# Optimization experiments

Hardware: AMD Instinct MI355X
Metric: run time of the kernel (lower is better)

## Reference

```python
import jax, jax.numpy as jnp
import numpy as np

E, B, F, L = 4, 8192, 2048, 100  # envs, batch/env, feature dim, num classes
LAM = 1.0  # hparams['RERM_lam']


def setup_inputs() -> dict:
    key = jax.random.key(0)
    k1, k2, k3 = jax.random.split(key, 3)
    feats = jax.random.normal(k1, (E, B, F), jnp.float32)
    y = jax.random.randint(k2, (E, B), 0, L)
    W = jax.random.normal(k3, (F, L), jnp.float32) * 0.02
    b = jnp.zeros((L,), jnp.float32)
    return {"feats": feats, "y": y, "W": W, "b": b}


def _rerm_loss(feats, y, W, b):
    # --- per-(label, env) masked means (mean_table / visit_table) ---
    onehot = jax.nn.one_hot(y, L, dtype=feats.dtype)          # [E,B,L]
    counts = onehot.sum(axis=1)                               # [E,L]
    sums = jnp.einsum('ebl,ebf->elf', onehot, feats)          # [E,L,F]
    means = sums / jnp.maximum(counts, 1.0)[..., None]        # [E,L,F]
    visit = (counts > 0).astype(feats.dtype)                  # [E,L]

    # --- torch.var(mean_table[i, fetch_envs, :], dim=1): variance over
    # feature dim per env (unbiased, /(F-1)), then mean over visited envs ---
    mu = means.mean(axis=-1, keepdims=True)                   # [E,L,1]
    var = jnp.sum((means - mu) ** 2, axis=-1) / (F - 1)       # [E,L]

    nvis = visit.sum(axis=0)                                  # [L]
    sel = (nvis > 1.5).astype(feats.dtype)                    # labels with >1 env
    per_label = (var * visit).sum(axis=0) / jnp.maximum(nvis, 1.0)  # [L]
    nzlabel = jnp.maximum(sel.sum(), 1.0)
    mean_loss = LAM * jnp.sum(per_label * sel) / nzlabel

    # --- cross-entropy over all envs concatenated ---
    logits = feats.reshape(E * B, F) @ W + b                  # [E*B,L]
    logp = jax.nn.log_softmax(logits, axis=-1)
    ce = -jnp.take_along_axis(logp, y.reshape(-1, 1), axis=1).mean()

    return mean_loss + ce


def reference(feats, y, W, b):
    return _rerm_loss(feats, y, W, b)
```

## Files before the change

### kernel.cpp

```cpp
#include <hip/hip_runtime.h>
#include <hip/hip_bf16.h>
#include <math.h>

#define E 4
#define B 8192
#define F 2048
#define L 100
#define NROWS (E * B)
#define LAMBDA 1.0f

typedef __attribute__((ext_vector_type(8))) short bf16x8;
typedef __attribute__((ext_vector_type(4))) float f32x4;

static __device__ inline unsigned short f2bf(float x) {
    unsigned u = __float_as_uint(x);
    unsigned r = (u + 0x7FFFu + ((u >> 16) & 1u)) >> 16;
    return (unsigned short)r;
}

__global__ void __launch_bounds__(256) k_prep(const float* __restrict__ W,
                                              unsigned short* __restrict__ Wt) {
    int g = blockIdx.x * 256 + threadIdx.x;
    int n = g >> 9;
    int k = (g & 511) * 4;
    ushort4 v;
    if (n < L) {
        v.x = f2bf(W[(size_t)(k + 0) * L + n]);
        v.y = f2bf(W[(size_t)(k + 1) * L + n]);
        v.z = f2bf(W[(size_t)(k + 2) * L + n]);
        v.w = f2bf(W[(size_t)(k + 3) * L + n]);
    } else {
        v.x = v.y = v.z = v.w = 0;
    }
    *(ushort4*)&Wt[(size_t)n * F + k] = v;
}

#define SG 4
#define NSG 25
#define SBS 8
#define SRW (B / SBS)

__global__ void __launch_bounds__(512) k_sums(const float* __restrict__ feats,
                                              const int* __restrict__ y,
                                              float* __restrict__ sums,
                                              int* __restrict__ counts) {
    __shared__ int ys[SRW];
    __shared__ unsigned short lists[SG][SRW];
    __shared__ int cnt[SG];
    int bi = blockIdx.x;
    int lg = bi % NSG;
    int bs = (bi / NSG) % SBS;
    int e  = bi / (NSG * SBS);
    int t = threadIdx.x;
    int lab0 = lg * SG;

    if (t < SG) cnt[t] = 0;
    const int* yb = y + e * B + bs * SRW;
    ys[t] = yb[t];
    ys[t + 512] = yb[t + 512];
    __syncthreads();

    for (int r = t; r < SRW; r += 512) {
        int lb = ys[r] - lab0;
        if ((unsigned)lb < SG) {
            int p = atomicAdd(&cnt[lb], 1);
            lists[lb][p] = (unsigned short)r;
        }
    }
    __syncthreads();

    const float* fb = feats + ((size_t)e * B + (size_t)bs * SRW) * F + t * 4;
#pragma unroll
    for (int lb = 0; lb < SG; ++lb) {
        int n = cnt[lb];
        float4 a0 = make_float4(0.f, 0.f, 0.f, 0.f);
        float4 a1 = make_float4(0.f, 0.f, 0.f, 0.f);
        int i = 0;
        for (; i + 2 <= n; i += 2) {
            int r0 = lists[lb][i];
            int r1 = lists[lb][i + 1];
            float4 x0 = *(const float4*)(fb + (size_t)r0 * F);
            float4 x1 = *(const float4*)(fb + (size_t)r1 * F);
            a0.x += x0.x; a0.y += x0.y; a0.z += x0.z; a0.w += x0.w;
            a1.x += x1.x; a1.y += x1.y; a1.z += x1.z; a1.w += x1.w;
        }
        if (i < n) {
            int r0 = lists[lb][i];
            float4 x0 = *(const float4*)(fb + (size_t)r0 * F);
            a0.x += x0.x; a0.y += x0.y; a0.z += x0.z; a0.w += x0.w;
        }
        if (n > 0) {
            float4 s;
            s.x = a0.x + a1.x; s.y = a0.y + a1.y;
            s.z = a0.z + a1.z; s.w = a0.w + a1.w;
            float* dst = sums + ((size_t)e * L + lab0 + lb) * F + t * 4;
            atomicAdd(dst + 0, s.x);
            atomicAdd(dst + 1, s.y);
            atomicAdd(dst + 2, s.z);
            atomicAdd(dst + 3, s.w);
        }
    }
    if (t < SG) atomicAdd(&counts[e * L + lab0 + t], cnt[t]);
}

__global__ void k_var(const float* __restrict__ sums,
                      const int* __restrict__ counts,
                      float* __restrict__ var_out) {
    int el = blockIdx.x;
    int t = threadIdx.x;
    float inv = 1.f / fmaxf((float)counts[el], 1.f);
    float sm = 0.f, sm2 = 0.f;
    for (int f = t; f < F; f += 256) {
        float m = sums[(size_t)el * F + f] * inv;
        sm += m; sm2 += m * m;
    }
    __shared__ float r1[256], r2[256];
    r1[t] = sm; r2[t] = sm2;
    __syncthreads();
    for (int s = 128; s > 0; s >>= 1) {
        if (t < s) { r1[t] += r1[t + s]; r2[t] += r2[t + s]; }
        __syncthreads();
    }
    if (t == 0) {
        float S = r1[0], S2 = r2[0];
        var_out[el] = (S2 - S * S / (float)F) / (float)(F - 1);
    }
}

#define GBM 128
#define GKC 64
#define APAD 72

__global__ void __launch_bounds__(512) k_gemm_ce(const float* __restrict__ feats,
                                                 const unsigned short* __restrict__ Wt,
                                                 const float* __restrict__ bias,
                                                 const int* __restrict__ y,
                                                 float* __restrict__ ce_accum) {
    __shared__ __align__(16) unsigned short As[GBM * APAD];
    __shared__ __align__(16) unsigned short Ws[GBM * APAD];
    __shared__ float red[8];
    int t = threadIdx.x;
    int wave = t >> 6, lane = t & 63;
    int quad = lane >> 4, l16 = lane & 15;
    size_t row0 = (size_t)blockIdx.x * GBM;

    f32x4 acc[8];
#pragma unroll
    for (int ct = 0; ct < 8; ++ct) acc[ct] = (f32x4){0.f, 0.f, 0.f, 0.f};

    int srow = t >> 2;
    int sq = t & 3;

    const float* aptr = feats + (row0 + srow) * (size_t)F + sq * 16;
    const unsigned short* wptr = Wt + (size_t)srow * F + sq * 16;

    float4 pa[4];
    uint4 pw[2];
#pragma unroll
    for (int i = 0; i < 4; ++i) pa[i] = ((const float4*)aptr)[i];
#pragma unroll
    for (int i = 0; i < 2; ++i) pw[i] = ((const uint4*)wptr)[i];

    for (int k0 = 0; k0 < F; k0 += GKC) {
        bf16x8 o0, o1;
        o0[0] = f2bf(pa[0].x); o0[1] = f2bf(pa[0].y); o0[2] = f2bf(pa[0].z); o0[3] = f2bf(pa[0].w);
        o0[4] = f2bf(pa[1].x); o0[5] = f2bf(pa[1].y); o0[6] = f2bf(pa[1].z); o0[7] = f2bf(pa[1].w);
        o1[0] = f2bf(pa[2].x); o1[1] = f2bf(pa[2].y); o1[2] = f2bf(pa[2].z); o1[3] = f2bf(pa[2].w);
        o1[4] = f2bf(pa[3].x); o1[5] = f2bf(pa[3].y); o1[6] = f2bf(pa[3].z); o1[7] = f2bf(pa[3].w);
        *(bf16x8*)&As[srow * APAD + sq * 16] = o0;
        *(bf16x8*)&As[srow * APAD + sq * 16 + 8] = o1;
        *(uint4*)&Ws[srow * APAD + sq * 16] = pw[0];
        *(uint4*)&Ws[srow * APAD + sq * 16 + 8] = pw[1];
        __syncthreads();

        if (k0 + GKC < F) {
            const float* ap = aptr + k0 + GKC;
            const unsigned short* wp = wptr + k0 + GKC;
#pragma unroll
            for (int i = 0; i < 4; ++i) pa[i] = ((const float4*)ap)[i];
#pragma unroll
            for (int i = 0; i < 2; ++i) pw[i] = ((const uint4*)wp)[i];
        }

#pragma unroll
        for (int ks = 0; ks < 2; ++ks) {
            bf16x8 bfr = *(const bf16x8*)&As[(wave * 16 + l16) * APAD + ks * 32 + quad * 8];
#pragma unroll
            for (int ct = 0; ct < 8; ++ct) {
                bf16x8 af = *(const bf16x8*)&Ws[(ct * 16 + l16) * APAD + ks * 32 + quad * 8];
                acc[ct] = __builtin_amdgcn_mfma_f32_16x16x32_bf16(af, bfr, acc[ct], 0, 0, 0);
            }
        }
        __syncthreads();
    }

    int grow = (int)row0 + wave * 16 + l16;
    int lab = y[grow];
    float vv[8][4];
    float vm = -1e30f;
#pragma unroll
    for (int ct = 0; ct < 8; ++ct) {
#pragma unroll
        for (int r = 0; r < 4; ++r) {
            int c = ct * 16 + quad * 4 + r;
            float bb = (c < L) ? bias[c] : 0.f;
            float v = acc[ct][r] + bb;
            vv[ct][r] = v;
            if (c < L) vm = fmaxf(vm, v);
        }
    }
    vm = fmaxf(vm, __shfl_xor(vm, 16));
    vm = fmaxf(vm, __shfl_xor(vm, 32));
    float se = 0.f;
    float tv = 0.f;
#pragma unroll
    for (int ct = 0; ct < 8; ++ct) {
#pragma unroll
        for (int r = 0; r < 4; ++r) {
            int c = ct * 16 + quad * 4 + r;
            if (c < L) se += __expf(vv[ct][r] - vm);
            if (c == lab) tv = vv[ct][r];
        }
    }
    se += __shfl_xor(se, 16);
    se += __shfl_xor(se, 32);
    tv += __shfl_xor(tv, 16);
    tv += __shfl_xor(tv, 32);
    float ce = vm + __logf(se) - tv;
#pragma unroll
    for (int s = 1; s <= 8; s <<= 1) ce += __shfl_xor(ce, s);
    if (lane == 0) red[wave] = ce;
    __syncthreads();
    if (t == 0) {
        float v = 0.f;
#pragma unroll
        for (int w = 0; w < 8; ++w) v += red[w];
        atomicAdd(ce_accum, v);
    }
}

__global__ void k_final(const int* __restrict__ counts,
                        const float* __restrict__ var_in,
                        const float* __restrict__ ce_accum,
                        float* __restrict__ out) {
    __shared__ float s_sum[128], s_cnt[128];
    int t = threadIdx.x;
    float selsum = 0.f, selcnt = 0.f;
    for (int l = t; l < L; l += 128) {
        float nvis = 0.f, vsum = 0.f;
        for (int e = 0; e < E; ++e) {
            if (counts[e * L + l] > 0) { nvis += 1.f; vsum += var_in[e * L + l]; }
        }
        float per_label = vsum / fmaxf(nvis, 1.f);
        if (nvis > 1.5f) { selsum += per_label; selcnt += 1.f; }
    }
    s_sum[t] = selsum; s_cnt[t] = selcnt;
    __syncthreads();
    for (int s = 64; s > 0; s >>= 1) {
        if (t < s) { s_sum[t] += s_sum[t + s]; s_cnt[t] += s_cnt[t + s]; }
        __syncthreads();
    }
    if (t == 0) {
        float mean_loss = LAMBDA * s_sum[0] / fmaxf(s_cnt[0], 1.f);
        float ce = ce_accum[0] / (float)NROWS;
        out[0] = mean_loss + ce;
    }
}

extern "C" void kernel_launch(void* const* d_in, const int* in_sizes, int n_in,
                              void* d_out, int out_size, void* d_ws, size_t ws_size,
                              hipStream_t stream) {
    const float* feats = (const float*)d_in[0];
    const int*   y     = (const int*)d_in[1];
    const float* Wm    = (const float*)d_in[2];
    const float* bias  = (const float*)d_in[3];
    float* out = (float*)d_out;

    char* ws = (char*)d_ws;
    float*          ce_accum = (float*)ws;
    int*            counts   = (int*)(ws + 256);
    float*          var_buf  = (float*)(ws + 2048);
    float*          sums     = (float*)(ws + 4096);
    unsigned short* Wt       = (unsigned short*)(ws + 4096 + (size_t)E * L * F * 4);

    hipMemsetAsync(ce_accum, 0, sizeof(float), stream);
    hipMemsetAsync(counts, 0, E * L * sizeof(int), stream);
    hipMemsetAsync(sums, 0, (size_t)E * L * F * sizeof(float), stream);

    k_prep<<<256, 256, 0, stream>>>(Wm, Wt);
    k_sums<<<E * SBS * NSG, 512, 0, stream>>>(feats, y, sums, counts);
    k_gemm_ce<<<NROWS / GBM, 512, 0, stream>>>(feats, Wt, bias, y, ce_accum);
    k_var<<<E * L, 256, 0, stream>>>(sums, counts, var_buf);
    k_final<<<1, 128, 0, stream>>>(counts, var_buf, ce_accum, out);
}
```

Measured before the change: 476.8 us.

## Fuse class-sum and GEMM-CE kernels into one launch, drop float atomics

Merges the per-label feature-sum kernel and the GEMM+cross-entropy kernel into a single launch whose blocks branch by index, so both stream feats concurrently. The sum blocks now write per-slice partial sums instead of doing float atomics into a zeroed buffer, which also removes the large memset. k_var reduces the 8 partials itself. The GEMM's padded class columns are trimmed from 128 to 112, cutting one MFMA column tile. This costs a larger workspace and more reads in k_var, and mixing the two block types may unbalance the schedule.

```diff
diff --git a/kernel.cpp b/kernel.cpp
--- a/kernel.cpp
+++ b/kernel.cpp
@@ -17,6 +17,18 @@
     unsigned r = (u + 0x7FFFu + ((u >> 16) & 1u)) >> 16;
     return (unsigned short)r;
 }
+
+#define SG 4
+#define NSG 25
+#define SBS 8
+#define SRW (B / SBS)
+#define NSUM (E * SBS * NSG)
+
+#define GBM 128
+#define GNC 112
+#define GKC 64
+#define APAD 72
+#define NGEMM (NROWS / GBM)
 
 __global__ void __launch_bounds__(256) k_prep(const float* __restrict__ W,
                                               unsigned short* __restrict__ Wt) {
@@ -35,83 +47,190 @@
     *(ushort4*)&Wt[(size_t)n * F + k] = v;
 }
 
-#define SG 4
-#define NSG 25
-#define SBS 8
-#define SRW (B / SBS)
-
-__global__ void __launch_bounds__(512) k_sums(const float* __restrict__ feats,
-                                              const int* __restrict__ y,
-                                              float* __restrict__ sums,
-                                              int* __restrict__ counts) {
-    __shared__ int ys[SRW];
-    __shared__ unsigned short lists[SG][SRW];
-    __shared__ int cnt[SG];
-    int bi = blockIdx.x;
-    int lg = bi % NSG;
-    int bs = (bi / NSG) % SBS;
-    int e  = bi / (NSG * SBS);
+__global__ void __launch_bounds__(512, 4) k_main(const float* __restrict__ feats,
+                                                 const int* __restrict__ y,
+                                                 const unsigned short* __restrict__ Wt,
+                                                 const float* __restrict__ bias,
+                                                 float* __restrict__ partial,
+                                                 int* __restrict__ counts,
+                                                 float* __restrict__ ce_accum) {
+    __shared__ __align__(16) char sm[34624];
     int t = threadIdx.x;
-    int lab0 = lg * SG;
-
-    if (t < SG) cnt[t] = 0;
-    const int* yb = y + e * B + bs * SRW;
-    ys[t] = yb[t];
-    ys[t + 512] = yb[t + 512];
-    __syncthreads();
-
-    for (int r = t; r < SRW; r += 512) {
-        int lb = ys[r] - lab0;
-        if ((unsigned)lb < SG) {
-            int p = atomicAdd(&cnt[lb], 1);
-            lists[lb][p] = (unsigned short)r;
-        }
-    }
-    __syncthreads();
-
-    const float* fb = feats + ((size_t)e * B + (size_t)bs * SRW) * F + t * 4;
-#pragma unroll
-    for (int lb = 0; lb < SG; ++lb) {
-        int n = cnt[lb];
-        float4 a0 = make_float4(0.f, 0.f, 0.f, 0.f);
-        float4 a1 = make_float4(0.f, 0.f, 0.f, 0.f);
-        int i = 0;
-        for (; i + 2 <= n; i += 2) {
-            int r0 = lists[lb][i];
-            int r1 = lists[lb][i + 1];
-            float4 x0 = *(const float4*)(fb + (size_t)r0 * F);
-            float4 x1 = *(const float4*)(fb + (size_t)r1 * F);
-            a0.x += x0.x; a0.y += x0.y; a0.z += x0.z; a0.w += x0.w;
-            a1.x += x1.x; a1.y += x1.y; a1.z += x1.z; a1.w += x1.w;
-        }
-        if (i < n) {
-            int r0 = lists[lb][i];
-            float4 x0 = *(const float4*)(fb + (size_t)r0 * F);
-            a0.x += x0.x; a0.y += x0.y; a0.z += x0.z; a0.w += x0.w;
-        }
-        if (n > 0) {
+
+    if (blockIdx.x < NGEMM) {
+        unsigned short* As = (unsigned short*)sm;
+        unsigned short* Ws = As + GBM * APAD;
+        float* red = (float*)(sm + 34560);
+        int wave = t >> 6, lane = t & 63;
+        int quad = lane >> 4, l16 = lane & 15;
+        size_t row0 = (size_t)blockIdx.x * GBM;
+
+        f32x4 acc[7];
+#pragma unroll
+        for (int ct = 0; ct < 7; ++ct) acc[ct] = (f32x4){0.f, 0.f, 0.f, 0.f};
+
+        int srow = t >> 2;
+        int sq = t & 3;
+
+        const float* aptr = feats + (row0 + srow) * (size_t)F + sq * 16;
+        const unsigned short* wptr = Wt + (size_t)srow * F + sq * 16;
+
+        float4 pa[4];
+        uint4 pw[2];
+#pragma unroll
+        for (int i = 0; i < 4; ++i) pa[i] = ((const float4*)aptr)[i];
+        if (srow < GNC) {
+#pragma unroll
+            for (int i = 0; i < 2; ++i) pw[i] = ((const uint4*)wptr)[i];
+        }
+
+        for (int k0 = 0; k0 < F; k0 += GKC) {
+            bf16x8 o0, o1;
+            o0[0] = f2bf(pa[0].x); o0[1] = f2bf(pa[0].y); o0[2] = f2bf(pa[0].z); o0[3] = f2bf(pa[0].w);
+            o0[4] = f2bf(pa[1].x); o0[5] = f2bf(pa[1].y); o0[6] = f2bf(pa[1].z); o0[7] = f2bf(pa[1].w);
+            o1[0] = f2bf(pa[2].x); o1[1] = f2bf(pa[2].y); o1[2] = f2bf(pa[2].z); o1[3] = f2bf(pa[2].w);
+            o1[4] = f2bf(pa[3].x); o1[5] = f2bf(pa[3].y); o1[6] = f2bf(pa[3].z); o1[7] = f2bf(pa[3].w);
+            *(bf16x8*)&As[srow * APAD + sq * 16] = o0;
+            *(bf16x8*)&As[srow * APAD + sq * 16 + 8] = o1;
+            if (srow < GNC) {
+                *(uint4*)&Ws[srow * APAD + sq * 16] = pw[0];
+                *(uint4*)&Ws[srow * APAD + sq * 16 + 8] = pw[1];
+            }
+            __syncthreads();
+
+            if (k0 + GKC < F) {
+                const float* ap = aptr + k0 + GKC;
+                const unsigned short* wp = wptr + k0 + GKC;
+#pragma unroll
+                for (int i = 0; i < 4; ++i) pa[i] = ((const float4*)ap)[i];
+                if (srow < GNC) {
+#pragma unroll
+                    for (int i = 0; i < 2; ++i) pw[i] = ((const uint4*)wp)[i];
+                }
+            }
+
+#pragma unroll
+            for (int ks = 0; ks < 2; ++ks) {
+                bf16x8 bfr = *(const bf16x8*)&As[(wave * 16 + l16) * APAD + ks * 32 + quad * 8];
+#pragma unroll
+                for (int ct = 0; ct < 7; ++ct) {
+                    bf16x8 af = *(const bf16x8*)&Ws[(ct * 16 + l16) * APAD + ks * 32 + quad * 8];
+                    acc[ct] = __builtin_amdgcn_mfma_f32_16x16x32_bf16(af, bfr, acc[ct], 0, 0, 0);
+                }
+            }
+            __syncthreads();
+        }
+
+        int grow = (int)row0 + wave * 16 + l16;
+        int lab = y[grow];
+        float vv[7][4];
+        float vm = -1e30f;
+#pragma unroll
+        for (int ct = 0; ct < 7; ++ct) {
+#pragma unroll
+            for (int r = 0; r < 4; ++r) {
+                int c = ct * 16 + quad * 4 + r;
+                float bb = (c < L) ? bias[c] : 0.f;
+                float v = acc[ct][r] + bb;
+                vv[ct][r] = v;
+                if (c < L) vm = fmaxf(vm, v);
+            }
+        }
+        vm = fmaxf(vm, __shfl_xor(vm, 16));
+        vm = fmaxf(vm, __shfl_xor(vm, 32));
+        float se = 0.f, tv = 0.f;
+#pragma unroll
+        for (int ct = 0; ct < 7; ++ct) {
+#pragma unroll
+            for (int r = 0; r < 4; ++r) {
+                int c = ct * 16 + quad * 4 + r;
+                if (c < L) se += __expf(vv[ct][r] - vm);
+                if (c == lab) tv = vv[ct][r];
+            }
+        }
+        se += __shfl_xor(se, 16);
+        se += __shfl_xor(se, 32);
+        tv += __shfl_xor(tv, 16);
+        tv += __shfl_xor(tv, 32);
+        float ce = vm + __logf(se) - tv;
+#pragma unroll
+        for (int s = 1; s <= 8; s <<= 1) ce += __shfl_xor(ce, s);
+        if (lane == 0) red[wave] = ce;
+        __syncthreads();
+        if (t == 0) {
+            float v = 0.f;
+#pragma unroll
+            for (int w = 0; w < 8; ++w) v += red[w];
+            atomicAdd(ce_accum, v);
+        }
+    } else {
+        int* ys = (int*)sm;
+        unsigned short (*lists)[SRW] = (unsigned short (*)[SRW])(sm + 4096);
+        int* cnt = (int*)(sm + 4096 + 8192);
+        int bi = blockIdx.x - NGEMM;
+        int lg = bi % NSG;
+        int bs = (bi / NSG) % SBS;
+        int e  = bi / (NSG * SBS);
+        int lab0 = lg * SG;
+
+        if (t < SG) cnt[t] = 0;
+        const int* yb = y + e * B + bs * SRW;
+        ys[t] = yb[t];
+        ys[t + 512] = yb[t + 512];
+        __syncthreads();
+
+        for (int r = t; r < SRW; r += 512) {
+            int lb = ys[r] - lab0;
+            if ((unsigned)lb < SG) {
+                int p = atomicAdd(&cnt[lb], 1);
+                lists[lb][p] = (unsigned short)r;
+            }
+        }
+        __syncthreads();
+
+        const float* fb = feats + ((size_t)e * B + (size_t)bs * SRW) * F + t * 4;
+#pragma unroll
+        for (int lb = 0; lb < SG; ++lb) {
+            int n = cnt[lb];
+            float4 a0 = make_float4(0.f, 0.f, 0.f, 0.f);
+            float4 a1 = make_float4(0.f, 0.f, 0.f, 0.f);
+            int i = 0;
+            for (; i + 2 <= n; i += 2) {
+                int r0 = lists[lb][i];
+                int r1 = lists[lb][i + 1];
+                float4 x0 = *(const float4*)(fb + (size_t)r0 * F);
+                float4 x1 = *(const float4*)(fb + (size_t)r1 * F);
+                a0.x += x0.x; a0.y += x0.y; a0.z += x0.z; a0.w += x0.w;
+                a1.x += x1.x; a1.y += x1.y; a1.z += x1.z; a1.w += x1.w;
+            }
+            if (i < n) {
+                int r0 = lists[lb][i];
+                float4 x0 = *(const float4*)(fb + (size_t)r0 * F);
+                a0.x += x0.x; a0.y += x0.y; a0.z += x0.z; a0.w += x0.w;
+            }
             float4 s;
             s.x = a0.x + a1.x; s.y = a0.y + a1.y;
             s.z = a0.z + a1.z; s.w = a0.w + a1.w;
-            float* dst = sums + ((size_t)e * L + lab0 + lb) * F + t * 4;
-            atomicAdd(dst + 0, s.x);
-            atomicAdd(dst + 1, s.y);
-            atomicAdd(dst + 2, s.z);
-            atomicAdd(dst + 3, s.w);
-        }
-    }
-    if (t < SG) atomicAdd(&counts[e * L + lab0 + t], cnt[t]);
-}
-
-__global__ void k_var(const float* __restrict__ sums,
+            *(float4*)&partial[(((size_t)e * SBS + bs) * L + lab0 + lb) * F + t * 4] = s;
+        }
+        if (t < SG) atomicAdd(&counts[e * L + lab0 + t], cnt[t]);
+    }
+}
+
+__global__ void k_var(const float* __restrict__ partial,
                       const int* __restrict__ counts,
                       float* __restrict__ var_out) {
     int el = blockIdx.x;
+    int e = el / L, l = el % L;
     int t = threadIdx.x;
     float inv = 1.f / fmaxf((float)counts[el], 1.f);
     float sm = 0.f, sm2 = 0.f;
     for (int f = t; f < F; f += 256) {
-        float m = sums[(size_t)el * F + f] * inv;
+        float s = 0.f;
+#pragma unroll
+        for (int bs = 0; bs < SBS; ++bs)
+            s += partial[(((size_t)e * SBS + bs) * L + l) * F + f];
+        float m = s * inv;
         sm += m; sm2 += m * m;
     }
     __shared__ float r1[256], r2[256];
@@ -124,118 +243,6 @@
     if (t == 0) {
         float S = r1[0], S2 = r2[0];
         var_out[el] = (S2 - S * S / (float)F) / (float)(F - 1);
-    }
-}
-
-#define GBM 128
-#define GKC 64
-#define APAD 72
-
-__global__ void __launch_bounds__(512) k_gemm_ce(const float* __restrict__ feats,
-                                                 const unsigned short* __restrict__ Wt,
-                                                 const float* __restrict__ bias,
-                                                 const int* __restrict__ y,
-                                                 float* __restrict__ ce_accum) {
-    __shared__ __align__(16) unsigned short As[GBM * APAD];
-    __shared__ __align__(16) unsigned short Ws[GBM * APAD];
-    __shared__ float red[8];
-    int t = threadIdx.x;
-    int wave = t >> 6, lane = t & 63;
-    int quad = lane >> 4, l16 = lane & 15;
-    size_t row0 = (size_t)blockIdx.x * GBM;
-
-    f32x4 acc[8];
-#pragma unroll
-    for (int ct = 0; ct < 8; ++ct) acc[ct] = (f32x4){0.f, 0.f, 0.f, 0.f};
-
-    int srow = t >> 2;
-    int sq = t & 3;
-
-    const float* aptr = feats + (row0 + srow) * (size_t)F + sq * 16;
-    const unsigned short* wptr = Wt + (size_t)srow * F + sq * 16;
-
-    float4 pa[4];
-    uint4 pw[2];
-#pragma unroll
-    for (int i = 0; i < 4; ++i) pa[i] = ((const float4*)aptr)[i];
-#pragma unroll
-    for (int i = 0; i < 2; ++i) pw[i] = ((const uint4*)wptr)[i];
-
-    for (int k0 = 0; k0 < F; k0 += GKC) {
-        bf16x8 o0, o1;
-        o0[0] = f2bf(pa[0].x); o0[1] = f2bf(pa[0].y); o0[2] = f2bf(pa[0].z); o0[3] = f2bf(pa[0].w);
-        o0[4] = f2bf(pa[1].x); o0[5] = f2bf(pa[1].y); o0[6] = f2bf(pa[1].z); o0[7] = f2bf(pa[1].w);
-        o1[0] = f2bf(pa[2].x); o1[1] = f2bf(pa[2].y); o1[2] = f2bf(pa[2].z); o1[3] = f2bf(pa[2].w);
-        o1[4] = f2bf(pa[3].x); o1[5] = f2bf(pa[3].y); o1[6] = f2bf(pa[3].z); o1[7] = f2bf(pa[3].w);
-        *(bf16x8*)&As[srow * APAD + sq * 16] = o0;
-        *(bf16x8*)&As[srow * APAD + sq * 16 + 8] = o1;
-        *(uint4*)&Ws[srow * APAD + sq * 16] = pw[0];
-        *(uint4*)&Ws[srow * APAD + sq * 16 + 8] = pw[1];
-        __syncthreads();
-
-        if (k0 + GKC < F) {
-            const float* ap = aptr + k0 + GKC;
-            const unsigned short* wp = wptr + k0 + GKC;
-#pragma unroll
-            for (int i = 0; i < 4; ++i) pa[i] = ((const float4*)ap)[i];
-#pragma unroll
-            for (int i = 0; i < 2; ++i) pw[i] = ((const uint4*)wp)[i];
-        }
-
-#pragma unroll
-        for (int ks = 0; ks < 2; ++ks) {
-            bf16x8 bfr = *(const bf16x8*)&As[(wave * 16 + l16) * APAD + ks * 32 + quad * 8];
-#pragma unroll
-            for (int ct = 0; ct < 8; ++ct) {
-                bf16x8 af = *(const bf16x8*)&Ws[(ct * 16 + l16) * APAD + ks * 32 + quad * 8];
-                acc[ct] = __builtin_amdgcn_mfma_f32_16x16x32_bf16(af, bfr, acc[ct], 0, 0, 0);
-            }
-        }
-        __syncthreads();
-    }
-
-    int grow = (int)row0 + wave * 16 + l16;
-    int lab = y[grow];
-    float vv[8][4];
-    float vm = -1e30f;
-#pragma unroll
-    for (int ct = 0; ct < 8; ++ct) {
-#pragma unroll
-        for (int r = 0; r < 4; ++r) {
-            int c = ct * 16 + quad * 4 + r;
-            float bb = (c < L) ? bias[c] : 0.f;
-            float v = acc[ct][r] + bb;
-            vv[ct][r] = v;
-            if (c < L) vm = fmaxf(vm, v);
-        }
-    }
-    vm = fmaxf(vm, __shfl_xor(vm, 16));
-    vm = fmaxf(vm, __shfl_xor(vm, 32));
-    float se = 0.f;
-    float tv = 0.f;
-#pragma unroll
-    for (int ct = 0; ct < 8; ++ct) {
-#pragma unroll
-        for (int r = 0; r < 4; ++r) {
-            int c = ct * 16 + quad * 4 + r;
-            if (c < L) se += __expf(vv[ct][r] - vm);
-            if (c == lab) tv = vv[ct][r];
-        }
-    }
-    se += __shfl_xor(se, 16);
-    se += __shfl_xor(se, 32);
-    tv += __shfl_xor(tv, 16);
-    tv += __shfl_xor(tv, 32);
-    float ce = vm + __logf(se) - tv;
-#pragma unroll
-    for (int s = 1; s <= 8; s <<= 1) ce += __shfl_xor(ce, s);
-    if (lane == 0) red[wave] = ce;
-    __syncthreads();
-    if (t == 0) {
-        float v = 0.f;
-#pragma unroll
-        for (int w = 0; w < 8; ++w) v += red[w];
-        atomicAdd(ce_accum, v);
     }
 }
 
@@ -280,16 +287,14 @@
     float*          ce_accum = (float*)ws;
     int*            counts   = (int*)(ws + 256);
     float*          var_buf  = (float*)(ws + 2048);
-    float*          sums     = (float*)(ws + 4096);
-    unsigned short* Wt       = (unsigned short*)(ws + 4096 + (size_t)E * L * F * 4);
+    float*          partial  = (float*)(ws + 4096);
+    unsigned short* Wt       = (unsigned short*)(ws + 4096 + (size_t)E * SBS * L * F * 4);
 
     hipMemsetAsync(ce_accum, 0, sizeof(float), stream);
     hipMemsetAsync(counts, 0, E * L * sizeof(int), stream);
-    hipMemsetAsync(sums, 0, (size_t)E * L * F * sizeof(float), stream);
-
-    k_prep<<<256, 256, 0, stream>>>(Wm, Wt);
-    k_sums<<<E * SBS * NSG, 512, 0, stream>>>(feats, y, sums, counts);
-    k_gemm_ce<<<NROWS / GBM, 512, 0, stream>>>(feats, Wt, bias, y, ce_accum);
-    k_var<<<E * L, 256, 0, stream>>>(sums, counts, var_buf);
+
+    k_prep<<<(GNC * 512) / 256, 256, 0, stream>>>(Wm, Wt);
+    k_main<<<NGEMM + NSUM, 512, 0, stream>>>(feats, y, Wt, bias, partial, counts, ce_accum);
+    k_var<<<E * L, 256, 0, stream>>>(partial, counts, var_buf);
     k_final<<<1, 128, 0, stream>>>(counts, var_buf, ce_accum, out);
 }
```

After: 438.3 us. -8.1%, faster.
